# Performance work log

Hardware: AMD Instinct MI355X
Metric: run time of the kernel (lower is better)

The kernel has to match this reference:

```python
import jax, jax.numpy as jnp
import numpy as np

B, T, U, V1 = 8, 256, 64, 1024  # V1 = vocab_size + 1 (blank at index 0)
BLANK = 0


def setup_inputs() -> dict:
    key = jax.random.key(0)
    k1, k2, k3, k4 = jax.random.split(key, 4)
    logits = jax.random.normal(k1, (B, T, U + 1, V1), jnp.float32)
    logit_lens = jax.random.randint(k2, (B,), T // 2, T + 1, jnp.int32)
    # target labels must never be the blank index (0)
    y = jax.random.randint(k3, (B, U), 1, V1, jnp.int32)
    y_lens = jax.random.randint(k4, (B,), U // 2, U + 1, jnp.int32)
    return {"logits": logits, "logit_lens": logit_lens, "y": y, "y_lens": y_lens}


def _rnnt_loss(logits, logit_lens, y, y_lens):
    """RNN-Transducer loss (forward-variable DP), reduction='mean' as in warprnnt."""
    b_, t_, u1, _ = logits.shape
    u_ = u1 - 1
    lp = jax.nn.log_softmax(logits, axis=-1)           # [B,T,U+1,V1]
    lp_blank = lp[..., BLANK]                          # [B,T,U+1]
    idx = jnp.broadcast_to(y[:, None, :, None], (b_, t_, u_, 1)).astype(jnp.int32)
    lp_label = jnp.take_along_axis(lp[:, :, :u_, :], idx, axis=3)[..., 0]  # [B,T,U]

    # alpha[0, u] = sum_{k<u} lp_label[0, k]
    alpha0 = jnp.concatenate(
        [jnp.zeros((b_, 1), lp.dtype), jnp.cumsum(lp_label[:, 0, :], axis=1)], axis=1
    )  # [B, U+1]

    def tstep(alpha_prev, xs):
        blank_prev, lab_t = xs                  # [B,U+1], [B,U]
        fb = alpha_prev + blank_prev            # come-from-blank term

        def ustep(carry, uxs):
            fb_u, lab_u = uxs                   # [B], [B]
            new = jnp.logaddexp(fb_u, carry + lab_u)
            return new, new

        _, rest = jax.lax.scan(ustep, fb[:, 0], (fb[:, 1:].T, lab_t.T))  # [U,B]
        alpha_new = jnp.concatenate([fb[:, :1], rest.T], axis=1)         # [B,U+1]
        return alpha_new, alpha_new

    xs = (jnp.moveaxis(lp_blank[:, :-1, :], 1, 0), jnp.moveaxis(lp_label[:, 1:, :], 1, 0))
    _, alphas = jax.lax.scan(tstep, alpha0, xs)          # [T-1,B,U+1]
    all_alpha = jnp.concatenate([alpha0[None], alphas], axis=0)  # [T,B,U+1]

    b_idx = jnp.arange(b_)
    t_idx = logit_lens.astype(jnp.int32) - 1
    u_idx = y_lens.astype(jnp.int32)
    log_like = all_alpha[t_idx, b_idx, u_idx] + lp_blank[b_idx, t_idx, u_idx]
    return -jnp.mean(log_like)


def reference(logits, logit_lens, y, y_lens):
    return _rnnt_loss(logits.astype(jnp.float32), logit_lens, y, y_lens)
```

## Files before the change

### kernel.cpp

```cpp
#include <hip/hip_runtime.h>
#include <math.h>

#define BB 8
#define TT 256
#define UU 64
#define U1 65
#define VV 1024

#define DD 320
#define BSTRIDE_BLANK (DD*U1)
#define BSTRIDE_LAB   (DD*UU)

__global__ __launch_bounds__(256) void k_rowsoftmax(
    const float* __restrict__ logits,
    const int* __restrict__ y,
    float* __restrict__ blankD,
    float* __restrict__ labD)
{
    const int lane = threadIdx.x & 63;
    const int r = (blockIdx.x * blockDim.x + threadIdx.x) >> 6;
    const int b   = r / (TT * U1);
    const int rem = r - b * (TT * U1);
    const int t   = rem / U1;
    const int u   = rem - t * U1;

    const float* row = logits + (size_t)r * VV;

    float labv = 0.f;
    if (lane == 0 && u < UU) {
        int yidx = y[b * UU + u];
        labv = row[yidx];
    }

    const float4* row4 = (const float4*)row;
    float4 x0 = row4[lane];
    float4 x1 = row4[lane + 64];
    float4 x2 = row4[lane + 128];
    float4 x3 = row4[lane + 192];

    float m = fmaxf(fmaxf(fmaxf(x0.x, x0.y), fmaxf(x0.z, x0.w)),
                    fmaxf(fmaxf(x1.x, x1.y), fmaxf(x1.z, x1.w)));
    m = fmaxf(m, fmaxf(fmaxf(fmaxf(x2.x, x2.y), fmaxf(x2.z, x2.w)),
                       fmaxf(fmaxf(x3.x, x3.y), fmaxf(x3.z, x3.w))));
    #pragma unroll
    for (int off = 32; off; off >>= 1)
        m = fmaxf(m, __shfl_xor(m, off));

    float s = __expf(x0.x - m) + __expf(x0.y - m) + __expf(x0.z - m) + __expf(x0.w - m)
            + __expf(x1.x - m) + __expf(x1.y - m) + __expf(x1.z - m) + __expf(x1.w - m)
            + __expf(x2.x - m) + __expf(x2.y - m) + __expf(x2.z - m) + __expf(x2.w - m)
            + __expf(x3.x - m) + __expf(x3.y - m) + __expf(x3.z - m) + __expf(x3.w - m);
    #pragma unroll
    for (int off = 32; off; off >>= 1)
        s += __shfl_xor(s, off);

    const float lse = m + __logf(s);

    if (lane == 0) {
        const int d = t + u;
        blankD[b * BSTRIDE_BLANK + d * U1 + u] = x0.x - lse;
        if (u < UU)
            labD[b * BSTRIDE_LAB + d * UU + u] = labv - lse;
    }
}

__device__ __forceinline__ float logaddexpf_(float a, float b) {
    float m = fmaxf(a, b);
    float d = fabsf(a - b);
    return m + log1pf(__expf(-d));
}

__global__ __launch_bounds__(64) void k_dp(
    const float* __restrict__ blankD,
    const float* __restrict__ labD,
    const int* __restrict__ logit_lens,
    const int* __restrict__ y_lens,
    float* __restrict__ out)
{
    const int lane = threadIdx.x;
    const int b    = blockIdx.x;

    const float* pb = blankD + b * BSTRIDE_BLANK;
    const float* pl = labD   + b * BSTRIDE_LAB;

    const int t_idx = logit_lens[b] - 1;
    const int u_idx = y_lens[b];
    const int u     = lane + 1;
    const int dmax  = t_idx + u_idx;

    float cur = pl[lane * (UU + 1)];
    #pragma unroll
    for (int off = 1; off < 64; off <<= 1) {
        float tv = __shfl_up(cur, off);
        if (lane >= off) cur += tv;
    }

    float a0 = 0.f;
    const float fin_blank = pb[dmax * U1 + u_idx];
    float ll = 0.f;

    float blank_v = pb[1 * U1 + u];
    float lab_v   = pl[1 * UU + lane];
    float blank0  = pb[0];

    for (int d = 2; d <= dmax; ++d) {
        const float nblank  = pb[d * U1 + u];
        const float nlab    = pl[d * UU + lane];
        const float nblank0 = pb[(d - 1) * U1];

        a0 += blank0;

        float left = __shfl_up(cur, 1);
        if (lane == 0) left = a0;

        const int t = d - u;
        if (t >= 1 && t <= TT - 1)
            cur = logaddexpf_(cur + blank_v, left + lab_v);

        if (t == t_idx && lane == u_idx - 1)
            ll = cur + fin_blank;

        blank_v = nblank; lab_v = nlab; blank0 = nblank0;
    }

    if (lane == u_idx - 1)
        atomicAdd(out, -ll * (1.0f / BB));
}

extern "C" void kernel_launch(void* const* d_in, const int* in_sizes, int n_in,
                              void* d_out, int out_size, void* d_ws, size_t ws_size,
                              hipStream_t stream) {
    const float* logits     = (const float*)d_in[0];
    const int*   logit_lens = (const int*)d_in[1];
    const int*   y          = (const int*)d_in[2];
    const int*   y_lens     = (const int*)d_in[3];
    float*       out        = (float*)d_out;

    float* blankD = (float*)d_ws;
    float* labD   = blankD + BB * BSTRIDE_BLANK;

    hipMemsetAsync(out, 0, sizeof(float) * out_size, stream);

    const int rows = BB * TT * U1;
    k_rowsoftmax<<<rows / 4, 256, 0, stream>>>(logits, y, blankD, labD);
    k_dp<<<BB, 64, 0, stream>>>(blankD, labD, logit_lens, y_lens, out);
}
```

Before: 797.3 us.

## Prefetch DP inputs deeper, use base-2 logaddexp, and drop memset/atomic

```diff
diff --git a/kernel.cpp b/kernel.cpp
--- a/kernel.cpp
+++ b/kernel.cpp
@@ -10,6 +10,9 @@
 #define DD 320
 #define BSTRIDE_BLANK (DD*U1)
 #define BSTRIDE_LAB   (DD*UU)
+
+#define LOG2E 1.4426950408889634f
+#define LN2   0.6931471805599453f
 
 __global__ __launch_bounds__(256) void k_rowsoftmax(
     const float* __restrict__ logits,
@@ -58,27 +61,24 @@
 
     if (lane == 0) {
         const int d = t + u;
-        blankD[b * BSTRIDE_BLANK + d * U1 + u] = x0.x - lse;
+        blankD[b * BSTRIDE_BLANK + d * U1 + u] = (x0.x - lse) * LOG2E;
         if (u < UU)
-            labD[b * BSTRIDE_LAB + d * UU + u] = labv - lse;
+            labD[b * BSTRIDE_LAB + d * UU + u] = (labv - lse) * LOG2E;
     }
 }
 
-__device__ __forceinline__ float logaddexpf_(float a, float b) {
-    float m = fmaxf(a, b);
-    float d = fabsf(a - b);
-    return m + log1pf(__expf(-d));
-}
+#define PF 8
 
-__global__ __launch_bounds__(64) void k_dp(
+__global__ __launch_bounds__(512) void k_dp(
     const float* __restrict__ blankD,
     const float* __restrict__ labD,
     const int* __restrict__ logit_lens,
     const int* __restrict__ y_lens,
-    float* __restrict__ out)
+    float* __restrict__ out,
+    int out_floats)
 {
-    const int lane = threadIdx.x;
-    const int b    = blockIdx.x;
+    const int lane = threadIdx.x & 63;
+    const int b    = threadIdx.x >> 6;
 
     const float* pb = blankD + b * BSTRIDE_BLANK;
     const float* pl = labD   + b * BSTRIDE_LAB;
@@ -99,32 +99,59 @@
     const float fin_blank = pb[dmax * U1 + u_idx];
     float ll = 0.f;
 
-    float blank_v = pb[1 * U1 + u];
-    float lab_v   = pl[1 * UU + lane];
-    float blank0  = pb[0];
-
-    for (int d = 2; d <= dmax; ++d) {
-        const float nblank  = pb[d * U1 + u];
-        const float nlab    = pl[d * UU + lane];
-        const float nblank0 = pb[(d - 1) * U1];
-
-        a0 += blank0;
-
-        float left = __shfl_up(cur, 1);
-        if (lane == 0) left = a0;
-
-        const int t = d - u;
-        if (t >= 1 && t <= TT - 1)
-            cur = logaddexpf_(cur + blank_v, left + lab_v);
-
-        if (t == t_idx && lane == u_idx - 1)
-            ll = cur + fin_blank;
-
-        blank_v = nblank; lab_v = nlab; blank0 = nblank0;
+    float rb[PF], rl[PF], r0[PF];
+    #pragma unroll
+    for (int i = 0; i < PF; ++i) {
+        rb[i] = pb[(1 + i) * U1 + u];
+        rl[i] = pl[(1 + i) * UU + lane];
+        r0[i] = pb[i * U1];
     }
 
-    if (lane == u_idx - 1)
-        atomicAdd(out, -ll * (1.0f / BB));
+    const int niter = dmax - 1;
+    const int nout  = (niter + PF - 1) / PF;
+    int d = 2;
+    for (int blk = 0; blk < nout; ++blk) {
+        #pragma unroll
+        for (int i = 0; i < PF; ++i, ++d) {
+            int pr = d + PF - 1;
+            if (pr > DD - 1) pr = DD - 1;
+            const float nb = pb[pr * U1 + u];
+            const float nl = pl[pr * UU + lane];
+            const float n0 = pb[(pr - 1) * U1];
+
+            if (d <= dmax) {
+                a0 += r0[i];
+
+                float left = __shfl_up(cur, 1);
+                if (lane == 0) left = a0;
+
+                const int t = d - u;
+                if (t >= 1 && t <= TT - 1) {
+                    const float aa = cur  + rb[i];
+                    const float bv = left + rl[i];
+                    const float mm = fmaxf(aa, bv);
+                    const float df = fabsf(aa - bv);
+                    cur = mm + __log2f(1.0f + exp2f(-df));
+                }
+
+                if (t == t_idx && lane == u_idx - 1)
+                    ll = cur + fin_blank;
+            }
+            rb[i] = nb; rl[i] = nl; r0[i] = n0;
+        }
+    }
+
+    __shared__ float part[BB];
+    if (lane == u_idx - 1) part[b] = ll * LN2;
+    __syncthreads();
+    if (threadIdx.x == 0) {
+        float s = 0.f;
+        #pragma unroll
+        for (int i = 0; i < BB; ++i) s += part[i];
+        out[0] = -s * (1.0f / BB);
+    }
+    for (int i = 1 + (int)threadIdx.x; i < out_floats; i += 512)
+        out[i] = 0.f;
 }
 
 extern "C" void kernel_launch(void* const* d_in, const int* in_sizes, int n_in,
@@ -139,9 +166,7 @@
     float* blankD = (float*)d_ws;
     float* labD   = blankD + BB * BSTRIDE_BLANK;
 
-    hipMemsetAsync(out, 0, sizeof(float) * out_size, stream);
-
     const int rows = BB * TT * U1;
     k_rowsoftmax<<<rows / 4, 256, 0, stream>>>(logits, y, blankD, labD);
-    k_dp<<<BB, 64, 0, stream>>>(blankD, labD, logit_lens, y_lens, out);
+    k_dp<<<1, 512, 0, stream>>>(blankD, labD, logit_lens, y_lens, out, out_size);
 }
```

Result: faster. 729.2 us (-8.5%).
